# Optimization experiments

Hardware: AMD Instinct MI355X
Metric: run time of the kernel (lower is better)

Reference implementation:

```python
import jax, jax.numpy as jnp
import numpy as np

B, S, D, H = 8, 2048, 1024, 128  # batch, seq (== CONTEXT_WINDOW), embed dim, headspace


def setup_inputs() -> dict:
    key = jax.random.key(0)
    ks = jax.random.split(key, 7)
    scale = 1.0 / np.sqrt(D)
    return {
        "x": jax.random.normal(ks[0], (B, S, D), dtype=jnp.float32),
        "Wq": jax.random.normal(ks[1], (D, H), dtype=jnp.float32) * scale,
        "bq": jax.random.normal(ks[2], (H,), dtype=jnp.float32) * 0.01,
        "Wk": jax.random.normal(ks[3], (D, H), dtype=jnp.float32) * scale,
        "bk": jax.random.normal(ks[4], (H,), dtype=jnp.float32) * 0.01,
        "Wv": jax.random.normal(ks[5], (D, H), dtype=jnp.float32) * scale,
        "bv": jax.random.normal(ks[6], (H,), dtype=jnp.float32) * 0.01,
    }


def reference(x, Wq, bq, Wk, bk, Wv, bv):
    # x: [B, S, D]
    embedlen = x.shape[-1]
    q = x @ Wq + bq  # [B, S, H]
    k = x @ Wk + bk  # [B, S, H]
    v = x @ Wv + bv  # [B, S, H]
    # NOTE: original code MULTIPLIES by sqrt(embedlen) (embedlen = full embed dim) --
    # faithful reproduction of the source, not the standard 1/sqrt(head_dim).
    scale = jnp.sqrt(jnp.asarray(embedlen, dtype=x.dtype))
    scores = jnp.einsum("bsh,bth->bst", q, k) * scale  # [B, S, S]
    seqlen = x.shape[1]
    causal = jnp.tril(jnp.ones((seqlen, seqlen), dtype=bool))
    scores = jnp.where(causal, scores, -jnp.inf)
    attn = jax.nn.softmax(scores, axis=-1)
    return jnp.einsum("bst,bth->bsh", attn, v)  # [B, S, H]
```

## Files before the change

### kernel.cpp

```cpp
#include <hip/hip_runtime.h>
#include <math.h>

#define SEQ 2048
#define DIM 1024
#define HD  128
#define NB  8
#define M_TOT (NB * SEQ)

typedef __attribute__((ext_vector_type(8))) short   short8;
typedef __attribute__((ext_vector_type(4))) float   floatx4;

__device__ __forceinline__ unsigned short f2bf(float f) {
    unsigned u = __builtin_bit_cast(unsigned, f);
    u += 0x7FFFu + ((u >> 16) & 1u);
    return (unsigned short)(u >> 16);
}
__device__ __forceinline__ float bf2f(unsigned short h) {
    unsigned u = ((unsigned)h) << 16;
    return __builtin_bit_cast(float, u);
}
__device__ __forceinline__ void async16(const void* g, void* l) {
    __builtin_amdgcn_global_load_lds(
        (const __attribute__((address_space(1))) unsigned int*)g,
        (__attribute__((address_space(3))) unsigned int*)l, 16, 0, 0);
}

#define MFMA16(a, b, c) __builtin_amdgcn_mfma_f32_16x16x32_bf16((a), (b), (c), 0, 0, 0)

__global__ __launch_bounds__(256) void wt_prep(
    const float* __restrict__ Wq, const float* __restrict__ Wk, const float* __restrict__ Wv,
    unsigned short* __restrict__ Wth, unsigned short* __restrict__ Wtl)
{
    int idx = blockIdx.x * 256 + threadIdx.x;
    int k   = idx & 1023;
    int n   = (idx >> 10) & 127;
    int mat = idx >> 17;
    const float* W = (mat == 0) ? Wq : (mat == 1) ? Wk : Wv;
    float v = W[k * HD + n];
    unsigned short hi = f2bf(v);
    Wth[idx] = hi;
    Wtl[idx] = f2bf(v - bf2f(hi));
}

__global__ __launch_bounds__(1024, 4) void qkv_fused(
    const float* __restrict__ x,
    const unsigned short* __restrict__ Wth, const unsigned short* __restrict__ Wtl,
    const float* __restrict__ bq, const float* __restrict__ bk, const float* __restrict__ bv,
    unsigned short* __restrict__ Qh, unsigned short* __restrict__ Ql,
    unsigned short* __restrict__ Kh, unsigned short* __restrict__ Kl,
    unsigned short* __restrict__ Vt)
{
    __shared__ short lds[96 * 512];

    const int t    = threadIdx.x;
    const int lane = t & 63;
    const int w    = t >> 6;
    const int lrow = lane & 15;
    const int quad = lane >> 4;

    const int R0 = blockIdx.x * 64;
    const int mh = w & 1;
    const int nh = w >> 1;

    auto stageB = [&](int k0, int qb) {
        #pragma unroll
        for (int i = 0; i < 3; ++i) {
            int f = i * 16 + w;
            if (f < 40) {
                int p   = (f >= 24);
                int ff  = p ? (f - 24) : f;
                int mat = ff >> 3, nf = ff & 7;
                const unsigned short* src = (p ? Wtl : Wth) + (size_t)mat * (HD * DIM)
                    + (size_t)(nf * 16 + lrow) * DIM + k0 + quad * 8;
                async16(src, &lds[(qb * 48 + 8 + f) * 512 + lane * 8]);
            }
        }
    };

    const int arow = t >> 4;
    const int akk  = (t & 15) * 2;
    auto xload = [&](int k0) -> float2 {
        return *(const float2*)&x[(size_t)(R0 + arow) * DIM + k0 + akk];
    };
    auto stageA = [&](float2 xv, int qb) {
        unsigned short h0 = f2bf(xv.x), h1 = f2bf(xv.y);
        unsigned short l0 = f2bf(xv.x - bf2f(h0)), l1 = f2bf(xv.y - bf2f(h1));
        int mi = arow >> 4, lr = arow & 15, qd = akk >> 3, el = akk & 7;
        int base = (qb * 48 + mi * 2) * 512 + (qd * 16 + lr) * 8 + el;
        short2 hv; hv.x = (short)h0; hv.y = (short)h1;
        short2 lv; lv.x = (short)l0; lv.y = (short)l1;
        *(short2*)&lds[base]       = hv;
        *(short2*)&lds[base + 512] = lv;
    };

    floatx4 acc[2][3];
    const floatx4 zf = {0.f, 0.f, 0.f, 0.f};
    #pragma unroll
    for (int mi2 = 0; mi2 < 2; ++mi2)
        #pragma unroll
        for (int c = 0; c < 3; ++c) acc[mi2][c] = zf;

    float2 xn = xload(0);
    stageA(xn, 0);
    stageB(0, 0);
    xn = xload(32);

    for (int it = 0; it < 32; ++it) {
        __syncthreads();
        const int k0 = it * 32;
        const int q  = it & 1;

        if (it < 31) {
            stageB(k0 + 32, q ^ 1);
            stageA(xn, q ^ 1);
        }
        if (it < 30) xn = xload(k0 + 64);

        short8 a[2][2];
        #pragma unroll
        for (int mi2 = 0; mi2 < 2; ++mi2)
            #pragma unroll
            for (int p = 0; p < 2; ++p)
                a[mi2][p] = *(short8*)&lds[(q * 48 + (mh * 2 + mi2) * 2 + p) * 512 + lane * 8];

        short8 bhq = *(short8*)&lds[(q * 48 + 8 +  0 + nh) * 512 + lane * 8];
        short8 bhk = *(short8*)&lds[(q * 48 + 8 +  8 + nh) * 512 + lane * 8];
        short8 bhv = *(short8*)&lds[(q * 48 + 8 + 16 + nh) * 512 + lane * 8];
        short8 blq = *(short8*)&lds[(q * 48 + 8 + 24 + nh) * 512 + lane * 8];
        short8 blk = *(short8*)&lds[(q * 48 + 8 + 32 + nh) * 512 + lane * 8];

        #pragma unroll
        for (int mi2 = 0; mi2 < 2; ++mi2) {
            acc[mi2][0] = MFMA16(a[mi2][0], bhq, acc[mi2][0]);
            acc[mi2][1] = MFMA16(a[mi2][0], bhk, acc[mi2][1]);
            acc[mi2][2] = MFMA16(a[mi2][0], bhv, acc[mi2][2]);
            acc[mi2][0] = MFMA16(a[mi2][1], bhq, acc[mi2][0]);
            acc[mi2][1] = MFMA16(a[mi2][1], bhk, acc[mi2][1]);
            acc[mi2][0] = MFMA16(a[mi2][0], blq, acc[mi2][0]);
            acc[mi2][1] = MFMA16(a[mi2][0], blk, acc[mi2][1]);
        }
    }

    const int col = nh * 16 + lrow;
    const float bqv = bq[col], bkv = bk[col], bvv = bv[col];
    #pragma unroll
    for (int mi2 = 0; mi2 < 2; ++mi2) {
        #pragma unroll
        for (int reg = 0; reg < 4; ++reg) {
            int gm = R0 + (mh * 2 + mi2) * 16 + quad * 4 + reg;
            float vq = (acc[mi2][0][reg] + bqv) * 32.0f;
            unsigned short h = f2bf(vq);
            Qh[(size_t)gm * HD + col] = h;
            Ql[(size_t)gm * HD + col] = f2bf(vq - bf2f(h));
            float vk = acc[mi2][1][reg] + bkv;
            h = f2bf(vk);
            Kh[(size_t)gm * HD + col] = h;
            Kl[(size_t)gm * HD + col] = f2bf(vk - bf2f(h));
            float vv = acc[mi2][2][reg] + bvv;
            int b = gm >> 11, s = gm & 2047;
            Vt[((size_t)b * HD + col) * SEQ + s] = f2bf(vv);
        }
    }
}

__global__ __launch_bounds__(256) void flash_attn(
    const unsigned short* __restrict__ Qh, const unsigned short* __restrict__ Ql,
    const unsigned short* __restrict__ Kh, const unsigned short* __restrict__ Kl,
    const unsigned short* __restrict__ Vt, float* __restrict__ out,
    float* __restrict__ Opart, float* __restrict__ ML, int split)
{
    __shared__ short lds[52 * 512];

    const int t    = threadIdx.x;
    const int lane = t & 63;
    const int w    = t >> 6;
    const int lrow = lane & 15;
    const int quad = lane >> 4;

    const int idx = blockIdx.x;
    const int b   = idx & 7;
    const int h   = split ? ((idx >> 3) & 1) : 0;
    const int s   = split ? (63 - (idx >> 4)) : (63 - (idx >> 3));
    const int T   = (s + 2) >> 1;
    const int Th  = (T + 1) >> 1;
    const int t0  = split ? (h ? Th : 0) : 0;
    const int t1  = split ? (h ? T : Th) : T;

    if (split && t0 >= t1) {
        float* op = Opart + (size_t)idx * 4096;
        for (int i = t; i < 4096; i += 256) op[i] = 0.0f;
        if (t < 32) { ML[(idx * 32 + t) * 2] = -1e30f; ML[(idx * 32 + t) * 2 + 1] = 0.0f; }
        return;
    }

    const int mh = w & 1;
    const int kh = w >> 1;
    const int R  = s * 32 + mh * 16;

    const size_t kbase = (size_t)b * SEQ * HD;
    const size_t vbase = (size_t)b * HD * SEQ;

    short8 qf[4][2];
    #pragma unroll
    for (int kc = 0; kc < 4; ++kc) {
        size_t off = kbase + (size_t)(R + lrow) * HD + kc * 32 + quad * 8;
        qf[kc][0] = *(const short8*)(Qh + off);
        qf[kc][1] = *(const short8*)(Ql + off);
    }

    const floatx4 zf = {0.f, 0.f, 0.f, 0.f};
    floatx4 accO[8];
    #pragma unroll
    for (int i = 0; i < 8; ++i) accO[i] = zf;
    float m_[4] = {-1e30f, -1e30f, -1e30f, -1e30f};
    float l_[4] = {0.f, 0.f, 0.f, 0.f};

    for (int it = t0; it < t1; ++it) {
        const int j0 = it * 64;
        __syncthreads();
        #pragma unroll
        for (int i = 0; i < 12; ++i) {
            int id = w * 12 + i;
            const unsigned short* src;
            if (id < 32) {
                int nt = id >> 3, kc = (id >> 1) & 3, p = id & 1;
                src = (p ? Kl : Kh) + kbase
                    + (size_t)(j0 + nt * 16 + lrow) * HD + kc * 32 + quad * 8;
            } else {
                int v = id - 32, df = v >> 1, kc = v & 1;
                src = Vt + vbase + (size_t)(df * 16 + lrow) * SEQ
                    + j0 + kc * 32 + quad * 8;
            }
            async16(src, &lds[id * 512 + lane * 8]);
        }
        __syncthreads();

        floatx4 S[2] = {zf, zf};
        #pragma unroll
        for (int ntl = 0; ntl < 2; ++ntl) {
            int nt = kh * 2 + ntl;
            #pragma unroll
            for (int kc = 0; kc < 4; ++kc) {
                short8 khf = *(short8*)&lds[(nt * 8 + kc * 2 + 0) * 512 + lane * 8];
                short8 klf = *(short8*)&lds[(nt * 8 + kc * 2 + 1) * 512 + lane * 8];
                S[ntl] = MFMA16(qf[kc][0], khf, S[ntl]);
                S[ntl] = MFMA16(qf[kc][0], klf, S[ntl]);
                S[ntl] = MFMA16(qf[kc][1], khf, S[ntl]);
            }
        }
        if (j0 + kh * 32 + 31 > R) {
            #pragma unroll
            for (int ntl = 0; ntl < 2; ++ntl) {
                int key = j0 + (kh * 2 + ntl) * 16 + lrow;
                #pragma unroll
                for (int reg = 0; reg < 4; ++reg) {
                    if (key > R + quad * 4 + reg) S[ntl][reg] = -INFINITY;
                }
            }
        }
        float alpha[4];
        #pragma unroll
        for (int reg = 0; reg < 4; ++reg) {
            float mx = fmaxf(S[0][reg], S[1][reg]);
            #pragma unroll
            for (int hh = 1; hh < 16; hh <<= 1) mx = fmaxf(mx, __shfl_xor(mx, hh));
            float mnew = fmaxf(fmaxf(m_[reg], mx), -1e30f);
            alpha[reg] = __expf(m_[reg] - mnew);
            m_[reg] = mnew;
            float p0 = __expf(S[0][reg] - mnew);
            float p1 = __expf(S[1][reg] - mnew);
            S[0][reg] = p0; S[1][reg] = p1;
            float ls = p0 + p1;
            #pragma unroll
            for (int hh = 1; hh < 16; hh <<= 1) ls += __shfl_xor(ls, hh);
            l_[reg] = l_[reg] * alpha[reg] + ls;
        }
        #pragma unroll
        for (int i = 0; i < 8; ++i)
            #pragma unroll
            for (int reg = 0; reg < 4; ++reg) accO[i][reg] *= alpha[reg];

        #pragma unroll
        for (int ntl = 0; ntl < 2; ++ntl) {
            #pragma unroll
            for (int reg = 0; reg < 4; ++reg) {
                int kloc = ntl * 16 + lrow;
                int jj = kloc & 7, q2 = (kloc >> 3) & 3;
                int lane2 = (quad * 4 + reg) + (q2 << 4);
                lds[(48 + w) * 512 + lane2 * 8 + jj] = (short)f2bf(S[ntl][reg]);
            }
        }
        short8 pf = *(short8*)&lds[(48 + w) * 512 + lane * 8];
        #pragma unroll
        for (int df = 0; df < 8; ++df) {
            short8 vf = *(short8*)&lds[(32 + df * 2 + kh) * 512 + lane * 8];
            accO[df] = MFMA16(pf, vf, accO[df]);
        }
    }

    __syncthreads();
    float* fl   = (float*)lds;
    float* Obuf = fl;
    float* mlb  = fl + 4096;
    if (lrow == 0) {
        #pragma unroll
        for (int reg = 0; reg < 4; ++reg) {
            int row = quad * 4 + reg;
            mlb[((kh * 2 + mh) * 16 + row) * 2 + 0] = m_[reg];
            mlb[((kh * 2 + mh) * 16 + row) * 2 + 1] = l_[reg];
        }
    }
    __syncthreads();
    float myw[4], Mrow[4], Drow[4];
    #pragma unroll
    for (int reg = 0; reg < 4; ++reg) {
        int row = quad * 4 + reg;
        float mo  = mlb[(((1 - kh) * 2 + mh) * 16 + row) * 2 + 0];
        float lo_ = mlb[(((1 - kh) * 2 + mh) * 16 + row) * 2 + 1];
        float M = fmaxf(m_[reg], mo);
        float d = l_[reg] * __expf(m_[reg] - M) + lo_ * __expf(mo - M);
        Mrow[reg] = M; Drow[reg] = d;
        myw[reg] = split ? __expf(m_[reg] - M) : (__expf(m_[reg] - M) / d);
    }
    if (kh == 0) {
        #pragma unroll
        for (int df = 0; df < 8; ++df)
            #pragma unroll
            for (int reg = 0; reg < 4; ++reg)
                Obuf[(mh * 16 + quad * 4 + reg) * 128 + df * 16 + lrow] =
                    accO[df][reg] * myw[reg];
    }
    __syncthreads();
    if (kh == 1) {
        if (split) {
            float* op = Opart + (size_t)idx * 4096;
            #pragma unroll
            for (int df = 0; df < 8; ++df) {
                #pragma unroll
                for (int reg = 0; reg < 4; ++reg) {
                    int row = mh * 16 + quad * 4 + reg;
                    op[row * 128 + df * 16 + lrow] =
                        Obuf[row * 128 + df * 16 + lrow] + accO[df][reg] * myw[reg];
                }
            }
            if (lrow == 0) {
                #pragma unroll
                for (int reg = 0; reg < 4; ++reg) {
                    int row = mh * 16 + quad * 4 + reg;
                    ML[(idx * 32 + row) * 2 + 0] = Mrow[reg];
                    ML[(idx * 32 + row) * 2 + 1] = Drow[reg];
                }
            }
        } else {
            #pragma unroll
            for (int df = 0; df < 8; ++df) {
                #pragma unroll
                for (int reg = 0; reg < 4; ++reg) {
                    float v = Obuf[(mh * 16 + quad * 4 + reg) * 128 + df * 16 + lrow]
                            + accO[df][reg] * myw[reg];
                    size_t o = ((size_t)(b * SEQ + R + quad * 4 + reg)) * HD + df * 16 + lrow;
                    out[o] = v;
                }
            }
        }
    }
}

__global__ __launch_bounds__(256) void splitk_merge(
    const float* __restrict__ Opart, const float* __restrict__ ML,
    float* __restrict__ out)
{
    int tid = blockIdx.x * 256 + threadIdx.x;
    int row = tid >> 5, c4 = tid & 31;
    int b = row >> 11, r = row & 2047, s = r >> 5, rr = r & 31;
    int i0 = ((63 - s) << 4) + b;
    int i1 = i0 + 8;
    float m0 = ML[(i0 * 32 + rr) * 2], l0 = ML[(i0 * 32 + rr) * 2 + 1];
    float m1 = ML[(i1 * 32 + rr) * 2], l1 = ML[(i1 * 32 + rr) * 2 + 1];
    float M  = fmaxf(m0, m1);
    float w0 = __expf(m0 - M), w1 = __expf(m1 - M);
    float inv = 1.0f / (w0 * l0 + w1 * l1);
    float4 a  = *(const float4*)&Opart[((size_t)i0 * 32 + rr) * 128 + c4 * 4];
    float4 bb = *(const float4*)&Opart[((size_t)i1 * 32 + rr) * 128 + c4 * 4];
    float4 o;
    o.x = (w0 * a.x + w1 * bb.x) * inv;
    o.y = (w0 * a.y + w1 * bb.y) * inv;
    o.z = (w0 * a.z + w1 * bb.z) * inv;
    o.w = (w0 * a.w + w1 * bb.w) * inv;
    *(float4*)&out[(size_t)row * 128 + c4 * 4] = o;
}

extern "C" void kernel_launch(void* const* d_in, const int* in_sizes, int n_in,
                              void* d_out, int out_size, void* d_ws, size_t ws_size,
                              hipStream_t stream) {
    const float* x  = (const float*)d_in[0];
    const float* Wq = (const float*)d_in[1];
    const float* bq = (const float*)d_in[2];
    const float* Wk = (const float*)d_in[3];
    const float* bk = (const float*)d_in[4];
    const float* Wv = (const float*)d_in[5];
    const float* bv = (const float*)d_in[6];
    float* out = (float*)d_out;

    unsigned short* Qh  = (unsigned short*)d_ws;
    unsigned short* Ql  = Qh  + (size_t)M_TOT * HD;
    unsigned short* Kh  = Ql  + (size_t)M_TOT * HD;
    unsigned short* Kl  = Kh  + (size_t)M_TOT * HD;
    unsigned short* Vt  = Kl  + (size_t)M_TOT * HD;
    unsigned short* Wth = Vt  + (size_t)M_TOT * HD;
    unsigned short* Wtl = Wth + (size_t)3 * HD * DIM;
    float* Opart = (float*)(Wtl + (size_t)3 * HD * DIM);
    float* ML    = Opart + (size_t)1024 * 32 * 128;

    const size_t need = 22544384ULL + 16777216ULL + 262144ULL;
    const int split = (ws_size >= need) ? 1 : 0;

    wt_prep<<<(3 * HD * DIM) / 256, 256, 0, stream>>>(Wq, Wk, Wv, Wth, Wtl);
    qkv_fused<<<256, 1024, 0, stream>>>(x, Wth, Wtl, bq, bk, bv, Qh, Ql, Kh, Kl, Vt);
    flash_attn<<<split ? 1024 : 512, 256, 0, stream>>>(Qh, Ql, Kh, Kl, Vt, out, Opart, ML, split);
    if (split) splitk_merge<<<2048, 256, 0, stream>>>(Opart, ML, out);
}
```

Measured before the change: 227.5 us.

## Triple-buffer QKV projection LDS staging with explicit waitcnt barriers

Moves the QKV projection GEMM main loop from double-buffered to triple-buffered LDS, grows the shared buffer, and prefetches x two steps ahead. The full __syncthreads is replaced by hand-written s_waitcnt vmcnt/lgkmcnt plus s_barrier, so the async global-to-LDS loads can stay in flight across iterations. The aim is to hide global load latency behind the MFMA work. In exchange it uses more LDS, which can lower occupancy, and it relies on vmcnt values hand-counted per wave group, which may be wrong.

Result: no change. 231.8 us (+1.9%).

```diff
diff --git a/kernel.cpp b/kernel.cpp
--- a/kernel.cpp
+++ b/kernel.cpp
@@ -50,7 +50,7 @@
     unsigned short* __restrict__ Kh, unsigned short* __restrict__ Kl,
     unsigned short* __restrict__ Vt)
 {
-    __shared__ short lds[96 * 512];
+    __shared__ short lds[144 * 512];
 
     const int t    = threadIdx.x;
     const int lane = t & 63;
@@ -100,34 +100,19 @@
         #pragma unroll
         for (int c = 0; c < 3; ++c) acc[mi2][c] = zf;
 
-    float2 xn = xload(0);
-    stageA(xn, 0);
-    stageB(0, 0);
-    xn = xload(32);
-
-    for (int it = 0; it < 32; ++it) {
-        __syncthreads();
-        const int k0 = it * 32;
-        const int q  = it & 1;
-
-        if (it < 31) {
-            stageB(k0 + 32, q ^ 1);
-            stageA(xn, q ^ 1);
-        }
-        if (it < 30) xn = xload(k0 + 64);
-
+    auto compute = [&](int qb) {
         short8 a[2][2];
         #pragma unroll
         for (int mi2 = 0; mi2 < 2; ++mi2)
             #pragma unroll
             for (int p = 0; p < 2; ++p)
-                a[mi2][p] = *(short8*)&lds[(q * 48 + (mh * 2 + mi2) * 2 + p) * 512 + lane * 8];
-
-        short8 bhq = *(short8*)&lds[(q * 48 + 8 +  0 + nh) * 512 + lane * 8];
-        short8 bhk = *(short8*)&lds[(q * 48 + 8 +  8 + nh) * 512 + lane * 8];
-        short8 bhv = *(short8*)&lds[(q * 48 + 8 + 16 + nh) * 512 + lane * 8];
-        short8 blq = *(short8*)&lds[(q * 48 + 8 + 24 + nh) * 512 + lane * 8];
-        short8 blk = *(short8*)&lds[(q * 48 + 8 + 32 + nh) * 512 + lane * 8];
+                a[mi2][p] = *(short8*)&lds[(qb * 48 + (mh * 2 + mi2) * 2 + p) * 512 + lane * 8];
+
+        short8 bhq = *(short8*)&lds[(qb * 48 + 8 +  0 + nh) * 512 + lane * 8];
+        short8 bhk = *(short8*)&lds[(qb * 48 + 8 +  8 + nh) * 512 + lane * 8];
+        short8 bhv = *(short8*)&lds[(qb * 48 + 8 + 16 + nh) * 512 + lane * 8];
+        short8 blq = *(short8*)&lds[(qb * 48 + 8 + 24 + nh) * 512 + lane * 8];
+        short8 blk = *(short8*)&lds[(qb * 48 + 8 + 32 + nh) * 512 + lane * 8];
 
         #pragma unroll
         for (int mi2 = 0; mi2 < 2; ++mi2) {
@@ -139,7 +124,41 @@
             acc[mi2][0] = MFMA16(a[mi2][0], blq, acc[mi2][0]);
             acc[mi2][1] = MFMA16(a[mi2][0], blk, acc[mi2][1]);
         }
-    }
+    };
+
+    stageB(0, 0);
+    float2 xv0 = xload(0);
+    stageA(xv0, 0);
+    float2 xn0 = xload(32);
+    float2 xn1 = xload(64);
+
+    int qr = 0, qw = 1;
+    #pragma unroll 3
+    for (int it = 0; it < 31; ++it) {
+        const int k0 = it * 32;
+
+        stageB(k0 + 32, qw);
+        stageA(xn0, qw);
+        xn0 = xn1;
+        int kx = (k0 + 96 <= DIM - 32) ? (k0 + 96) : (DIM - 32);
+        xn1 = xload(kx);
+
+        if (w < 8) asm volatile("s_waitcnt vmcnt(5)" ::: "memory");
+        else       asm volatile("s_waitcnt vmcnt(4)" ::: "memory");
+        asm volatile("s_waitcnt lgkmcnt(0)" ::: "memory");
+        __builtin_amdgcn_s_barrier();
+        __builtin_amdgcn_sched_barrier(0);
+
+        compute(qr);
+
+        qr = (qr == 2) ? 0 : qr + 1;
+        qw = (qw == 2) ? 0 : qw + 1;
+    }
+    asm volatile("s_waitcnt vmcnt(0)" ::: "memory");
+    asm volatile("s_waitcnt lgkmcnt(0)" ::: "memory");
+    __builtin_amdgcn_s_barrier();
+    __builtin_amdgcn_sched_barrier(0);
+    compute(qr);
 
     const int col = nh * 16 + lrow;
     const float bqv = bq[col], bkv = bk[col], bvv = bv[col];
```

## Split QKV projection across output-column halves with smaller blocks and deeper x prefetch

Applied to the files above, without the earlier changes.

The QKV projection kernel now launches a 2D grid, with each block covering half of the 128 output columns, 512 threads per block, and a smaller LDS footprint. This doubles the block count to improve occupancy and CU coverage. The cost is that each block re-reads and re-splits the same x rows, so x traffic and conversion work double. The x load is widened to float4 and prefetched two steps ahead to hide global latency.

New measurement: 218.5 us. 1.04x faster.

```diff
diff --git a/kernel.cpp b/kernel.cpp
--- a/kernel.cpp
+++ b/kernel.cpp
@@ -8,6 +8,7 @@
 #define M_TOT (NB * SEQ)
 
 typedef __attribute__((ext_vector_type(8))) short   short8;
+typedef __attribute__((ext_vector_type(4))) short   short4v;
 typedef __attribute__((ext_vector_type(4))) float   floatx4;
 
 __device__ __forceinline__ unsigned short f2bf(float f) {
@@ -42,7 +43,7 @@
     Wtl[idx] = f2bf(v - bf2f(hi));
 }
 
-__global__ __launch_bounds__(1024, 4) void qkv_fused(
+__global__ __launch_bounds__(512, 4) void qkv_fused(
     const float* __restrict__ x,
     const unsigned short* __restrict__ Wth, const unsigned short* __restrict__ Wtl,
     const float* __restrict__ bq, const float* __restrict__ bk, const float* __restrict__ bv,
@@ -50,7 +51,7 @@
     unsigned short* __restrict__ Kh, unsigned short* __restrict__ Kl,
     unsigned short* __restrict__ Vt)
 {
-    __shared__ short lds[96 * 512];
+    __shared__ short lds[56 * 512];
 
     const int t    = threadIdx.x;
     const int lane = t & 63;
@@ -59,38 +60,43 @@
     const int quad = lane >> 4;
 
     const int R0 = blockIdx.x * 64;
+    const int z  = blockIdx.y;
     const int mh = w & 1;
     const int nh = w >> 1;
 
     auto stageB = [&](int k0, int qb) {
         #pragma unroll
         for (int i = 0; i < 3; ++i) {
-            int f = i * 16 + w;
-            if (f < 40) {
-                int p   = (f >= 24);
-                int ff  = p ? (f - 24) : f;
-                int mat = ff >> 3, nf = ff & 7;
+            int f = i * 8 + w;
+            if (f < 20) {
+                int p   = (f >= 12);
+                int ff  = p ? (f - 12) : f;
+                int mat = ff >> 2, nfl = ff & 3;
                 const unsigned short* src = (p ? Wtl : Wth) + (size_t)mat * (HD * DIM)
-                    + (size_t)(nf * 16 + lrow) * DIM + k0 + quad * 8;
-                async16(src, &lds[(qb * 48 + 8 + f) * 512 + lane * 8]);
+                    + (size_t)((z * 4 + nfl) * 16 + lrow) * DIM + k0 + quad * 8;
+                async16(src, &lds[(qb * 28 + 8 + f) * 512 + lane * 8]);
             }
         }
     };
 
-    const int arow = t >> 4;
-    const int akk  = (t & 15) * 2;
-    auto xload = [&](int k0) -> float2 {
-        return *(const float2*)&x[(size_t)(R0 + arow) * DIM + k0 + akk];
+    const int arow = t >> 3;
+    const int akk  = (t & 7) * 4;
+    auto xload = [&](int k0) -> float4 {
+        return *(const float4*)&x[(size_t)(R0 + arow) * DIM + k0 + akk];
     };
-    auto stageA = [&](float2 xv, int qb) {
-        unsigned short h0 = f2bf(xv.x), h1 = f2bf(xv.y);
-        unsigned short l0 = f2bf(xv.x - bf2f(h0)), l1 = f2bf(xv.y - bf2f(h1));
+    auto stageA = [&](float4 xv, int qb) {
+        float xf[4] = {xv.x, xv.y, xv.z, xv.w};
+        short4v hv, lv;
+        #pragma unroll
+        for (int j = 0; j < 4; ++j) {
+            unsigned short h = f2bf(xf[j]);
+            hv[j] = (short)h;
+            lv[j] = (short)f2bf(xf[j] - bf2f(h));
+        }
         int mi = arow >> 4, lr = arow & 15, qd = akk >> 3, el = akk & 7;
-        int base = (qb * 48 + mi * 2) * 512 + (qd * 16 + lr) * 8 + el;
-        short2 hv; hv.x = (short)h0; hv.y = (short)h1;
-        short2 lv; lv.x = (short)l0; lv.y = (short)l1;
-        *(short2*)&lds[base]       = hv;
-        *(short2*)&lds[base + 512] = lv;
+        int base = (qb * 28 + mi * 2) * 512 + (qd * 16 + lr) * 8 + el;
+        *(short4v*)&lds[base]       = hv;
+        *(short4v*)&lds[base + 512] = lv;
     };
 
     floatx4 acc[2][3];
@@ -100,34 +106,19 @@
         #pragma unroll
         for (int c = 0; c < 3; ++c) acc[mi2][c] = zf;
 
-    float2 xn = xload(0);
-    stageA(xn, 0);
-    stageB(0, 0);
-    xn = xload(32);
-
-    for (int it = 0; it < 32; ++it) {
-        __syncthreads();
-        const int k0 = it * 32;
-        const int q  = it & 1;
-
-        if (it < 31) {
-            stageB(k0 + 32, q ^ 1);
-            stageA(xn, q ^ 1);
-        }
-        if (it < 30) xn = xload(k0 + 64);
-
+    auto compute = [&](int qb) {
         short8 a[2][2];
         #pragma unroll
         for (int mi2 = 0; mi2 < 2; ++mi2)
             #pragma unroll
             for (int p = 0; p < 2; ++p)
-                a[mi2][p] = *(short8*)&lds[(q * 48 + (mh * 2 + mi2) * 2 + p) * 512 + lane * 8];
-
-        short8 bhq = *(short8*)&lds[(q * 48 + 8 +  0 + nh) * 512 + lane * 8];
-        short8 bhk = *(short8*)&lds[(q * 48 + 8 +  8 + nh) * 512 + lane * 8];
-        short8 bhv = *(short8*)&lds[(q * 48 + 8 + 16 + nh) * 512 + lane * 8];
-        short8 blq = *(short8*)&lds[(q * 48 + 8 + 24 + nh) * 512 + lane * 8];
-        short8 blk = *(short8*)&lds[(q * 48 + 8 + 32 + nh) * 512 + lane * 8];
+                a[mi2][p] = *(short8*)&lds[(qb * 28 + (mh * 2 + mi2) * 2 + p) * 512 + lane * 8];
+
+        short8 bhq = *(short8*)&lds[(qb * 28 + 8 +  0 + nh) * 512 + lane * 8];
+        short8 bhk = *(short8*)&lds[(qb * 28 + 8 +  4 + nh) * 512 + lane * 8];
+        short8 bhv = *(short8*)&lds[(qb * 28 + 8 +  8 + nh) * 512 + lane * 8];
+        short8 blq = *(short8*)&lds[(qb * 28 + 20 + 0 + nh) * 512 + lane * 8];
+        short8 blk = *(short8*)&lds[(qb * 28 + 20 + 4 + nh) * 512 + lane * 8];
 
         #pragma unroll
         for (int mi2 = 0; mi2 < 2; ++mi2) {
@@ -139,9 +130,30 @@
             acc[mi2][0] = MFMA16(a[mi2][0], blq, acc[mi2][0]);
             acc[mi2][1] = MFMA16(a[mi2][0], blk, acc[mi2][1]);
         }
-    }
-
-    const int col = nh * 16 + lrow;
+    };
+
+    stageB(0, 0);
+    stageA(xload(0), 0);
+    float4 xn0 = xload(32);
+    float4 xn1 = xload(64);
+
+    for (int it = 0; it < 32; ++it) {
+        __syncthreads();
+        const int k0 = it * 32;
+        const int q  = it & 1;
+
+        if (it < 31) {
+            stageB(k0 + 32, q ^ 1);
+            stageA(xn0, q ^ 1);
+            xn0 = xn1;
+            int kx = (k0 + 96 <= DIM - 32) ? (k0 + 96) : (DIM - 32);
+            xn1 = xload(kx);
+        }
+
+        compute(q);
+    }
+
+    const int col = (z * 4 + nh) * 16 + lrow;
     const float bqv = bq[col], bkv = bk[col], bvv = bv[col];
     #pragma unroll
     for (int mi2 = 0; mi2 < 2; ++mi2) {
@@ -416,7 +428,7 @@
     const int split = (ws_size >= need) ? 1 : 0;
 
     wt_prep<<<(3 * HD * DIM) / 256, 256, 0, stream>>>(Wq, Wk, Wv, Wth, Wtl);
-    qkv_fused<<<256, 1024, 0, stream>>>(x, Wth, Wtl, bq, bk, bv, Qh, Ql, Kh, Kl, Vt);
+    qkv_fused<<<dim3(256, 2), 512, 0, stream>>>(x, Wth, Wtl, bq, bk, bv, Qh, Ql, Kh, Kl, Vt);
     flash_attn<<<split ? 1024 : 512, 256, 0, stream>>>(Qh, Ql, Kh, Kl, Vt, out, Opart, ML, split);
     if (split) splitk_merge<<<2048, 256, 0, stream>>>(Opart, ML, out);
 }
```
